# Performance work log

Hardware: AMD Instinct MI355X
Metric: run time of the kernel (lower is better)

## Reference

```python
import jax, jax.numpy as jnp
import numpy as np


def setup_inputs() -> dict:
    key = jax.random.key(0)
    k_x, k_q, k_k, k_v = jax.random.split(key, 4)
    seq_len, d_in, d_out = 4096, 1024, 1024
    x = jax.random.normal(k_x, (seq_len, d_in), dtype=jnp.float32)
    # torch nn.Linear weights are [d_out, d_in]; applied as x @ W.T
    scale = 1.0 / np.sqrt(d_in)
    Wq = jax.random.uniform(k_q, (d_out, d_in), jnp.float32, -scale, scale)
    Wk = jax.random.uniform(k_k, (d_out, d_in), jnp.float32, -scale, scale)
    Wv = jax.random.uniform(k_v, (d_out, d_in), jnp.float32, -scale, scale)
    return {"x": x, "Wq": Wq, "Wk": Wk, "Wv": Wv}


def reference(x, Wq, Wk, Wv):
    # x: [S, d_in]; Wq/Wk/Wv: [d_out, d_in]
    queries = x @ Wq.T          # [S, d_out]
    keys = x @ Wk.T             # [S, d_out]
    values = x @ Wv.T           # [S, d_out]
    d_k = keys.shape[-1]
    attn_scores = queries @ keys.T                      # [S, S]
    attn_weights = jax.nn.softmax(attn_scores / jnp.sqrt(jnp.float32(d_k)), axis=-1)
    S = attn_scores.shape[0]
    tril = jnp.tril(jnp.ones((S, S), dtype=attn_weights.dtype))
    masked = tril * attn_weights
    masked_norm = masked / jnp.sum(masked, axis=-1, keepdims=True)
    context_vec = masked_norm @ values                  # [S, d_out]
    return context_vec
```

## Files before the change

kernel.cpp:

```cpp
#include <hip/hip_runtime.h>
#include <hip/hip_bf16.h>


typedef __bf16 bf16_t;
typedef __bf16 bf16x4v __attribute__((ext_vector_type(4)));
typedef __bf16 bf16x8 __attribute__((ext_vector_type(8)));
typedef float f32x4 __attribute__((ext_vector_type(4)));
typedef unsigned char u8;
typedef long long i64_t;

#define AS1 __attribute__((address_space(1)))
#define AS3 __attribute__((address_space(3)))
#define WAIT_VMCNT(N) asm volatile("s_waitcnt vmcnt(" #N ")" ::: "memory")
#define BARRIER_RAW() asm volatile("s_barrier" ::: "memory")

__device__ __forceinline__ void async_copy16(const void* g, void* l) {
    __builtin_amdgcn_global_load_lds((AS1 void*)(g), (AS3 void*)(l), 16, 0, 0);
}

__device__ __forceinline__ u8 f32_to_fp8(float v) {
    return (u8)(__builtin_amdgcn_cvt_pk_fp8_f32(v, v, 0, false) & 0xff);
}

__device__ __forceinline__ void store_conv(float* p, float v) { *p = v; }
__device__ __forceinline__ void store_conv(bf16_t* p, float v) { *p = (bf16_t)v; }
__device__ __forceinline__ void store_conv(u8* p, float v) { *p = f32_to_fp8(v); }

__device__ __forceinline__ float sum32(const float* p) {
    const f32x4* v = (const f32x4*)p;
    float s = 0.f;
#pragma unroll
    for (int u = 0; u < 8; ++u) {
        f32x4 a = v[u];
        s += a[0] + a[1] + a[2] + a[3];
    }
    return s;
}

template <int EPI, typename OutT>
__device__ __forceinline__ void gemm_tile_bf16(const bf16_t* __restrict__ A, int lda,
                                               const bf16_t* __restrict__ B, int ldb,
                                               OutT* __restrict__ C, int ldc,
                                               int kb0, int kb1, float alpha,
                                               char* __restrict__ smem,
                                               const float* __restrict__ inv) {
    constexpr int BK = 64;
    bf16_t* As = (bf16_t*)smem;
    bf16_t* Bs = (bf16_t*)(smem + 32768);
    const int tid = threadIdx.x;
    const int lane = tid & 63, wave = tid >> 6;
    const int wm = wave >> 1, wn = wave & 1;
    const int q = lane >> 4, l16 = lane & 15;

    f32x4 acc[4][4] = {};

    const bf16_t* aSrc[4];
    const bf16_t* bSrc[4];
    int ldsOff[4];
#pragma unroll
    for (int it = 0; it < 4; ++it) {
        int c = it * 256 + tid;
        int r = c >> 3, b = c & 7;
        int sb = b ^ (r & 7);
        aSrc[it] = A + (size_t)r * lda + sb * 8;
        bSrc[it] = B + (size_t)r * ldb + sb * 8;
        ldsOff[it] = c * 8;
    }

    {
        const int k0 = kb0 * BK;
#pragma unroll
        for (int it = 0; it < 4; ++it) async_copy16(aSrc[it] + k0, &As[ldsOff[it]]);
#pragma unroll
        for (int it = 0; it < 4; ++it) async_copy16(bSrc[it] + k0, &Bs[ldsOff[it]]);
    }

    int cur = 0;
    for (int kb = kb0; kb < kb1; ++kb) {
        if (kb + 1 < kb1) {
            const int k0 = (kb + 1) * BK;
            const int boff = (cur ^ 1) * 8192;
#pragma unroll
            for (int it = 0; it < 4; ++it) async_copy16(aSrc[it] + k0, &As[boff + ldsOff[it]]);
#pragma unroll
            for (int it = 0; it < 4; ++it) async_copy16(bSrc[it] + k0, &Bs[boff + ldsOff[it]]);
            WAIT_VMCNT(8);
        } else {
            WAIT_VMCNT(0);
        }
        __builtin_amdgcn_sched_barrier(0);
        BARRIER_RAW();
        const bf16_t* Ab = As + cur * 8192;
        const bf16_t* Bb = Bs + cur * 8192;
        __builtin_amdgcn_s_setprio(1);
#pragma unroll
        for (int k2 = 0; k2 < 2; ++k2) {
            bf16x8 af[4], bfr[4];
#pragma unroll
            for (int mt = 0; mt < 4; ++mt) {
                int m = wm * 64 + mt * 16 + l16;
                int blk = (k2 * 4 + q) ^ (m & 7);
                af[mt] = *(const bf16x8*)&Ab[m * BK + blk * 8];
            }
#pragma unroll
            for (int nt = 0; nt < 4; ++nt) {
                int nn = wn * 64 + nt * 16 + l16;
                int blk = (k2 * 4 + q) ^ (nn & 7);
                bfr[nt] = *(const bf16x8*)&Bb[nn * BK + blk * 8];
            }
#pragma unroll
            for (int mt = 0; mt < 4; ++mt)
#pragma unroll
                for (int nt = 0; nt < 4; ++nt)
                    acc[mt][nt] = __builtin_amdgcn_mfma_f32_16x16x32_bf16(
                        af[mt], bfr[nt], acc[mt][nt], 0, 0, 0);
        }
        __builtin_amdgcn_s_setprio(0);
        BARRIER_RAW();
        cur ^= 1;
    }

    constexpr int S = (int)sizeof(OutT);
    constexpr int RB = 128 * S;
    const int row0 = wm * 64, col0 = wn * 64;
#pragma unroll
    for (int mt = 0; mt < 4; ++mt)
#pragma unroll
        for (int nt = 0; nt < 4; ++nt)
#pragma unroll
            for (int r = 0; r < 4; ++r) {
                int lr = row0 + mt * 16 + q * 4 + r;
                int lc = col0 + nt * 16 + l16;
                float v = acc[mt][nt][r];
                v = (EPI == 2) ? v * inv[lr] : v * alpha;
                int cb = (lc * S) >> 4;
                int sw = cb ^ ((lr >> 2) & 7);
                store_conv((OutT*)(smem + lr * RB + (sw << 4) + ((lc * S) & 15)), v);
            }
    __syncthreads();
#pragma unroll
    for (int p = 0; p < 4 * S; ++p) {
        int g = p * 4096 + tid * 16;
        int r = g / RB;
        int wb = g & (RB - 1);
        int sc = (wb >> 4) ^ ((r >> 2) & 7);
        f32x4 val = *(const f32x4*)(smem + r * RB + (sc << 4));
        *(f32x4*)((char*)C + (size_t)r * ((size_t)ldc * S) + wb) = val;
    }
}

__device__ __forceinline__ void gemm_tile_bf16_sb(const bf16_t* __restrict__ A, int lda,
                                                  const bf16_t* __restrict__ B, int ldb,
                                                  bf16_t* __restrict__ C, int ldc,
                                                  int kb1, char* __restrict__ smem) {
    constexpr int BK = 64;
    bf16_t* As = (bf16_t*)smem;
    bf16_t* Bs = (bf16_t*)(smem + 16384);
    const int tid = threadIdx.x;
    const int lane = tid & 63, wave = tid >> 6;
    const int wm = wave >> 1, wn = wave & 1;
    const int q = lane >> 4, l16 = lane & 15;

    f32x4 acc[4][4] = {};

    const bf16_t* aSrc[4];
    const bf16_t* bSrc[4];
    int ldsOff[4];
#pragma unroll
    for (int it = 0; it < 4; ++it) {
        int c = it * 256 + tid;
        int r = c >> 3, b = c & 7;
        int sb = b ^ (r & 7);
        aSrc[it] = A + (size_t)r * lda + sb * 8;
        bSrc[it] = B + (size_t)r * ldb + sb * 8;
        ldsOff[it] = c * 8;
    }

    for (int kb = 0; kb < kb1; ++kb) {
        const int k0 = kb * BK;
#pragma unroll
        for (int it = 0; it < 4; ++it) async_copy16(aSrc[it] + k0, &As[ldsOff[it]]);
#pragma unroll
        for (int it = 0; it < 4; ++it) async_copy16(bSrc[it] + k0, &Bs[ldsOff[it]]);
        __syncthreads();
        __builtin_amdgcn_s_setprio(1);
#pragma unroll
        for (int k2 = 0; k2 < 2; ++k2) {
            bf16x8 af[4], bfr[4];
#pragma unroll
            for (int mt = 0; mt < 4; ++mt) {
                int m = wm * 64 + mt * 16 + l16;
                int blk = (k2 * 4 + q) ^ (m & 7);
                af[mt] = *(const bf16x8*)&As[m * BK + blk * 8];
            }
#pragma unroll
            for (int nt = 0; nt < 4; ++nt) {
                int nn = wn * 64 + nt * 16 + l16;
                int blk = (k2 * 4 + q) ^ (nn & 7);
                bfr[nt] = *(const bf16x8*)&Bs[nn * BK + blk * 8];
            }
#pragma unroll
            for (int mt = 0; mt < 4; ++mt)
#pragma unroll
                for (int nt = 0; nt < 4; ++nt)
                    acc[mt][nt] = __builtin_amdgcn_mfma_f32_16x16x32_bf16(
                        af[mt], bfr[nt], acc[mt][nt], 0, 0, 0);
        }
        __builtin_amdgcn_s_setprio(0);
        __syncthreads();
    }

    constexpr int RB = 256;
    const int row0 = wm * 64, col0 = wn * 64;
#pragma unroll
    for (int mt = 0; mt < 4; ++mt)
#pragma unroll
        for (int nt = 0; nt < 4; ++nt)
#pragma unroll
            for (int r = 0; r < 4; ++r) {
                int lr = row0 + mt * 16 + q * 4 + r;
                int lc = col0 + nt * 16 + l16;
                int cb = (lc * 2) >> 4;
                int sw = cb ^ ((lr >> 2) & 7);
                *(bf16_t*)(smem + lr * RB + (sw << 4) + ((lc * 2) & 15)) =
                    (bf16_t)acc[mt][nt][r];
            }
    __syncthreads();
#pragma unroll
    for (int p = 0; p < 8; ++p) {
        int g = p * 4096 + tid * 16;
        int r = g >> 8, wb = g & 255;
        int sc = (wb >> 4) ^ ((r >> 2) & 7);
        f32x4 val = *(const f32x4*)(smem + r * RB + (sc << 4));
        *(f32x4*)((char*)C + (size_t)r * ((size_t)ldc * 2) + wb) = val;
    }
}

__device__ __forceinline__ void scores_tile_fp8_sb(const u8* __restrict__ A, int lda,
                                                   const u8* __restrict__ B, int ldb,
                                                   bf16_t* __restrict__ C, int ldc,
                                                   float alpha, char* __restrict__ smem,
                                                   float* __restrict__ partial,
                                                   int gr0, int gc0) {
    u8* As = (u8*)smem;
    u8* Bs = (u8*)(smem + 16384);
    const int tid = threadIdx.x;
    const int lane = tid & 63, wave = tid >> 6;
    const int wm = wave >> 1, wn = wave & 1;
    const int q = lane >> 4, l16 = lane & 15;

    f32x4 acc[4][4] = {};

    const u8* aSrc[4];
    const u8* bSrc[4];
    int ldsOff[4];
#pragma unroll
    for (int it = 0; it < 4; ++it) {
        int c = it * 256 + tid;
        int r = c >> 3, b = c & 7;
        int sb = b ^ (r & 7);
        aSrc[it] = A + (size_t)r * lda + sb * 16;
        bSrc[it] = B + (size_t)r * ldb + sb * 16;
        ldsOff[it] = c * 16;
    }

    for (int kb = 0; kb < 8; ++kb) {
        const int k0 = kb * 128;
#pragma unroll
        for (int it = 0; it < 4; ++it) async_copy16(aSrc[it] + k0, &As[ldsOff[it]]);
#pragma unroll
        for (int it = 0; it < 4; ++it) async_copy16(bSrc[it] + k0, &Bs[ldsOff[it]]);
        __syncthreads();
        __builtin_amdgcn_s_setprio(1);
#pragma unroll
        for (int k2 = 0; k2 < 4; ++k2) {
            i64_t af[4], bfr[4];
            const int cb = 2 * k2 + (q >> 1), co = (q & 1) * 8;
#pragma unroll
            for (int mt = 0; mt < 4; ++mt) {
                int m = wm * 64 + mt * 16 + l16;
                af[mt] = *(const i64_t*)&As[m * 128 + ((cb ^ (m & 7)) << 4) + co];
            }
#pragma unroll
            for (int nt = 0; nt < 4; ++nt) {
                int nn = wn * 64 + nt * 16 + l16;
                bfr[nt] = *(const i64_t*)&Bs[nn * 128 + ((cb ^ (nn & 7)) << 4) + co];
            }
#pragma unroll
            for (int mt = 0; mt < 4; ++mt)
#pragma unroll
                for (int nt = 0; nt < 4; ++nt)
                    acc[mt][nt] = __builtin_amdgcn_mfma_f32_16x16x32_fp8_fp8(
                        af[mt], bfr[nt], acc[mt][nt], 0, 0, 0);
        }
        __builtin_amdgcn_s_setprio(0);
        __syncthreads();
    }

    float* sred = (float*)(smem + 32768);
    const int row0 = wm * 64, col0 = wn * 64;
    float esum[4][4];
#pragma unroll
    for (int mt = 0; mt < 4; ++mt)
#pragma unroll
        for (int r = 0; r < 4; ++r) esum[mt][r] = 0.f;
#pragma unroll
    for (int mt = 0; mt < 4; ++mt)
#pragma unroll
        for (int nt = 0; nt < 4; ++nt)
#pragma unroll
            for (int r = 0; r < 4; ++r) {
                int lr = row0 + mt * 16 + q * 4 + r;
                int lc = col0 + nt * 16 + l16;
                float pe = (gc0 + lc > gr0 + lr) ? 0.f : __expf(acc[mt][nt][r] * alpha);
                esum[mt][r] += pe;
                int sw = (lc >> 3) ^ ((lr >> 2) & 7);
                *(bf16_t*)(smem + lr * 256 + (sw << 4) + ((lc * 2) & 15)) = (bf16_t)pe;
            }
#pragma unroll
    for (int mt = 0; mt < 4; ++mt)
#pragma unroll
        for (int r = 0; r < 4; ++r) {
#pragma unroll
            for (int off = 1; off < 16; off <<= 1)
                esum[mt][r] += __shfl_xor(esum[mt][r], off, 64);
            if (l16 == 0) sred[(row0 + mt * 16 + q * 4 + r) * 2 + wn] = esum[mt][r];
        }
    __syncthreads();
#pragma unroll
    for (int p = 0; p < 8; ++p) {
        int g = p * 4096 + tid * 16;
        int r = g >> 8;
        int wb = g & 255;
        int sc = (wb >> 4) ^ ((r >> 2) & 7);
        f32x4 val = *(const f32x4*)(smem + r * 256 + (sc << 4));
        *(f32x4*)((char*)C + (size_t)r * ((size_t)ldc * 2) + wb) = val;
    }
    if (tid < 128) partial[(size_t)tid * 32] = sred[tid * 2] + sred[tid * 2 + 1];
}

__global__ __launch_bounds__(256) void k_qkv(const bf16_t* __restrict__ xb,
                                             const bf16_t* __restrict__ wqk,
                                             u8* __restrict__ qk) {
    __shared__ __attribute__((aligned(16))) char smem[65536];
    int b = blockIdx.x;
    int bm = b & 31, bn = b >> 5;
    gemm_tile_bf16<0, u8>(xb + (size_t)bm * 128 * 1024, 1024,
                          wqk + (size_t)bn * 128 * 1024, 1024,
                          qk + (size_t)bm * 128 * 2048 + bn * 128, 2048,
                          0, 16, 1.f, smem, nullptr);
}

__global__ __launch_bounds__(256, 4) void k_sv(const bf16_t* __restrict__ xb,
                                               const bf16_t* __restrict__ wvb,
                                               const u8* __restrict__ qk,
                                               bf16_t* __restrict__ vt,
                                               bf16_t* __restrict__ P,
                                               float* __restrict__ rowsum_part) {
    __shared__ __attribute__((aligned(16))) char smem[33792];
    int b = blockIdx.x;
    if (b < 256) {
        int bm = b & 7, bn = b >> 3;
        gemm_tile_bf16_sb(wvb + (size_t)bm * 128 * 1024, 1024,
                          xb + (size_t)bn * 128 * 1024, 1024,
                          vt + (size_t)bm * 128 * 4096 + bn * 128, 4096,
                          16, smem);
        return;
    }
    int t = b - 256;
    int bm = (int)((sqrtf(8.f * (float)t + 1.f) - 1.f) * 0.5f);
    while (bm * (bm + 1) / 2 > t) --bm;
    while ((bm + 1) * (bm + 2) / 2 <= t) ++bm;
    int bn = t - bm * (bm + 1) / 2;
    scores_tile_fp8_sb(qk + (size_t)bm * 128 * 2048, 2048,
                       qk + 1024 + (size_t)bn * 128 * 2048, 2048,
                       P + (size_t)bm * 128 * 4096 + bn * 128, 4096,
                       0.03125f, smem,
                       rowsum_part + (size_t)bm * 128 * 32 + bn,
                       bm * 128, bn * 128);
    if (bn == bm) {
        float* rp = rowsum_part + (size_t)bm * 128 * 32;
        int tid = threadIdx.x;
        for (int r = tid >> 4; r < 128; r += 16)
            for (int u = bm + 1 + (tid & 15); u < 32; u += 16)
                rp[r * 32 + u] = 0.f;
    }
}

__global__ __launch_bounds__(256) void k_pv(const bf16_t* __restrict__ P,
                                            const bf16_t* __restrict__ vt,
                                            const float* __restrict__ rowsum_part,
                                            float* __restrict__ out,
                                            float* __restrict__ partials) {
    __shared__ __attribute__((aligned(16))) char smem[65536];
    __shared__ float sInv[128];
    int b = blockIdx.x;
    int bn = b & 7, g = b >> 3;
    int bm, s, ns;
    if (g < 11)      { bm = g;                  s = 0;             ns = 1; }
    else if (g < 33) { bm = 11 + (g - 11) / 2;  s = (g - 11) % 2;  ns = 2; }
    else             { bm = 22 + (g - 33) / 3;  s = (g - 33) % 3;  ns = 3; }
    int nk = 2 * (bm + 1);
    int kb0 = s * nk / ns;
    int kb1 = (s + 1) * nk / ns;

    const bf16_t* A = P + (size_t)bm * 128 * 4096;
    const bf16_t* B = vt + (size_t)bn * 128 * 4096;
    if (ns == 1) {
        int tid = threadIdx.x;
        if (tid < 128)
            sInv[tid] = 1.f / sum32(rowsum_part + (size_t)(bm * 128 + tid) * 32);
        gemm_tile_bf16<2, float>(A, 4096, B, 4096,
                                 out + (size_t)bm * 128 * 1024 + bn * 128, 1024,
                                 kb0, kb1, 1.f, smem, sInv);
    } else {
        int cum = (bm < 22) ? (bm - 11) * 2 : 22 + (bm - 22) * 3;
        gemm_tile_bf16<0, float>(A, 4096, B, 4096,
                                 partials + ((size_t)(cum + s) * 8 + bn) * 16384, 128,
                                 kb0, kb1, 1.f, smem, nullptr);
    }
}

__global__ __launch_bounds__(256) void k_reduce(const float* __restrict__ partials,
                                                const float* __restrict__ rowsum_part,
                                                float* __restrict__ out) {
    int b = blockIdx.x;
    int t = b % 168, p = b / 168;
    int bm = 11 + t % 21, bn = t / 21;
    int ns = (bm < 22) ? 2 : 3;
    int cum = (bm < 22) ? (bm - 11) * 2 : 22 + (bm - 22) * 3;
    __shared__ float sInv[8];
    int tid = threadIdx.x;
    if (tid < 8) {
        int row = bm * 128 + p * 8 + tid;
        sInv[tid] = 1.f / sum32(rowsum_part + (size_t)row * 32);
    }
    __syncthreads();

    int idx = p * 1024 + tid * 4;
    int lr = idx >> 7, lc = idx & 127;
    float sx = 0.f, sy = 0.f, sz = 0.f, sw = 0.f;
    for (int u = 0; u < ns; ++u) {
        const float4 v = *(const float4*)(partials + ((size_t)(cum + u) * 8 + bn) * 16384 + idx);
        sx += v.x; sy += v.y; sz += v.z; sw += v.w;
    }
    float inv = sInv[lr - p * 8];
    float4 o = {sx * inv, sy * inv, sz * inv, sw * inv};
    *(float4*)(out + (size_t)(bm * 128 + lr) * 1024 + bn * 128 + lc) = o;
}

__global__ __launch_bounds__(256) void cast_to_bf16(const float* __restrict__ x,
                                                    const float* __restrict__ Wq,
                                                    const float* __restrict__ Wk,
                                                    const float* __restrict__ Wv,
                                                    bf16_t* __restrict__ xb,
                                                    bf16_t* __restrict__ wqk,
                                                    bf16_t* __restrict__ wv) {
    const int NX = (4096 * 1024) / 4;
    const int NW = (1024 * 1024) / 4;
    int idx = blockIdx.x * 256 + threadIdx.x;
    const float* src;
    bf16_t* dst;
    int off;
    if (idx < NX) {
        src = x; dst = xb; off = idx;
    } else if (idx < NX + NW) {
        src = Wq; dst = wqk; off = idx - NX;
    } else if (idx < NX + 2 * NW) {
        src = Wk; dst = wqk + (size_t)NW * 4; off = idx - NX - NW;
    } else {
        src = Wv; dst = wv; off = idx - NX - 2 * NW;
    }
    float4 f = ((const float4*)src)[off];
    bf16x4v o;
    o.x = (bf16_t)f.x; o.y = (bf16_t)f.y; o.z = (bf16_t)f.z; o.w = (bf16_t)f.w;
    *(bf16x4v*)(dst + (size_t)off * 4) = o;
}

extern "C" void kernel_launch(void* const* d_in, const int* in_sizes, int n_in,
                              void* d_out, int out_size, void* d_ws, size_t ws_size,
                              hipStream_t stream) {
    (void)in_sizes; (void)n_in; (void)out_size; (void)ws_size;
    const float* x  = (const float*)d_in[0];
    const float* Wq = (const float*)d_in[1];
    const float* Wk = (const float*)d_in[2];
    const float* Wv = (const float*)d_in[3];
    float* out = (float*)d_out;

    char* ws = (char*)d_ws;
    bf16_t* xb   = (bf16_t*)(ws + (size_t)0);
    bf16_t* wqk  = (bf16_t*)(ws + ((size_t)8 << 20));
    bf16_t* wvb  = (bf16_t*)(ws + ((size_t)12 << 20));
    u8*     qk   = (u8*)(ws + ((size_t)14 << 20));
    bf16_t* vt   = (bf16_t*)(ws + ((size_t)22 << 20));
    bf16_t* P    = (bf16_t*)(ws + ((size_t)30 << 20));
    float* rowsp = (float*)(ws + ((size_t)62 << 20));
    float* parts = (float*)(ws + ((size_t)64 << 20));

    cast_to_bf16<<<7168, 256, 0, stream>>>(x, Wq, Wk, Wv, xb, wqk, wvb);

    k_qkv<<<512, 256, 0, stream>>>(xb, wqk, qk);

    k_sv<<<784, 256, 0, stream>>>(xb, wvb, qk, vt, P, rowsp);

    k_pv<<<504, 256, 0, stream>>>(P, vt, rowsp, out, parts);
    k_reduce<<<2688, 256, 0, stream>>>(parts, rowsp, out);
}
```

Measured before the change: 165.6 us.

## Use single-buffered 32KB-LDS PV tile for higher occupancy and finer split-K

Adds a single-buffered bf16 GEMM tile for the P·V stage that uses about 33KB of LDS instead of 64KB, and writes the fp32 epilogue in two 64-row halves so it fits that buffer. Launch bounds now request 4 blocks per CU. The split-K schedule is rebalanced to use up to 4 splits for the longest causal rows, which raises the block count and the matching reduce grid. In exchange, the kernel loses the overlap that double buffering gave between loads and MFMA, and writes more partial sums to memory for the reduce pass.

```diff
diff --git a/kernel.cpp b/kernel.cpp
--- a/kernel.cpp
+++ b/kernel.cpp
@@ -233,6 +233,103 @@
         int sc = (wb >> 4) ^ ((r >> 2) & 7);
         f32x4 val = *(const f32x4*)(smem + r * RB + (sc << 4));
         *(f32x4*)((char*)C + (size_t)r * ((size_t)ldc * 2) + wb) = val;
+    }
+}
+
+template <int EPI>
+__device__ __forceinline__ void gemm_tile_f32_sb(const bf16_t* __restrict__ A, int lda,
+                                                 const bf16_t* __restrict__ B, int ldb,
+                                                 float* __restrict__ C, int ldc,
+                                                 int kb0, int kb1,
+                                                 char* __restrict__ smem,
+                                                 const float* __restrict__ inv) {
+    constexpr int BK = 64;
+    bf16_t* As = (bf16_t*)smem;
+    bf16_t* Bs = (bf16_t*)(smem + 16384);
+    const int tid = threadIdx.x;
+    const int lane = tid & 63, wave = tid >> 6;
+    const int wm = wave >> 1, wn = wave & 1;
+    const int q = lane >> 4, l16 = lane & 15;
+
+    f32x4 acc[4][4] = {};
+
+    const bf16_t* aSrc[4];
+    const bf16_t* bSrc[4];
+    int ldsOff[4];
+#pragma unroll
+    for (int it = 0; it < 4; ++it) {
+        int c = it * 256 + tid;
+        int r = c >> 3, b = c & 7;
+        int sb = b ^ (r & 7);
+        aSrc[it] = A + (size_t)r * lda + sb * 8;
+        bSrc[it] = B + (size_t)r * ldb + sb * 8;
+        ldsOff[it] = c * 8;
+    }
+
+    for (int kb = kb0; kb < kb1; ++kb) {
+        const int k0 = kb * BK;
+#pragma unroll
+        for (int it = 0; it < 4; ++it) async_copy16(aSrc[it] + k0, &As[ldsOff[it]]);
+#pragma unroll
+        for (int it = 0; it < 4; ++it) async_copy16(bSrc[it] + k0, &Bs[ldsOff[it]]);
+        __syncthreads();
+        __builtin_amdgcn_s_setprio(1);
+#pragma unroll
+        for (int k2 = 0; k2 < 2; ++k2) {
+            bf16x8 af[4], bfr[4];
+#pragma unroll
+            for (int mt = 0; mt < 4; ++mt) {
+                int m = wm * 64 + mt * 16 + l16;
+                int blk = (k2 * 4 + q) ^ (m & 7);
+                af[mt] = *(const bf16x8*)&As[m * BK + blk * 8];
+            }
+#pragma unroll
+            for (int nt = 0; nt < 4; ++nt) {
+                int nn = wn * 64 + nt * 16 + l16;
+                int blk = (k2 * 4 + q) ^ (nn & 7);
+                bfr[nt] = *(const bf16x8*)&Bs[nn * BK + blk * 8];
+            }
+#pragma unroll
+            for (int mt = 0; mt < 4; ++mt)
+#pragma unroll
+                for (int nt = 0; nt < 4; ++nt)
+                    acc[mt][nt] = __builtin_amdgcn_mfma_f32_16x16x32_bf16(
+                        af[mt], bfr[nt], acc[mt][nt], 0, 0, 0);
+        }
+        __builtin_amdgcn_s_setprio(0);
+        __syncthreads();
+    }
+
+    const int row0 = wm * 64, col0 = wn * 64;
+#pragma unroll
+    for (int hh = 0; hh < 2; ++hh) {
+        if (wm == hh) {
+#pragma unroll
+            for (int mt = 0; mt < 4; ++mt)
+#pragma unroll
+                for (int nt = 0; nt < 4; ++nt)
+#pragma unroll
+                    for (int r = 0; r < 4; ++r) {
+                        int lr = row0 + mt * 16 + q * 4 + r;
+                        int rl = lr & 63;
+                        int lc = col0 + nt * 16 + l16;
+                        float v = acc[mt][nt][r];
+                        if (EPI == 2) v *= inv[lr];
+                        int cb = lc >> 2;
+                        int sw = cb ^ ((rl >> 2) & 7);
+                        *(float*)(smem + rl * 512 + (sw << 4) + ((lc * 4) & 15)) = v;
+                    }
+        }
+        __syncthreads();
+#pragma unroll
+        for (int p = 0; p < 8; ++p) {
+            int g = p * 4096 + tid * 16;
+            int r = g >> 9, wb = g & 511;
+            int sc = (wb >> 4) ^ ((r >> 2) & 7);
+            f32x4 val = *(const f32x4*)(smem + r * 512 + (sc << 4));
+            *(f32x4*)&C[(size_t)(hh * 64 + r) * ldc + (wb >> 2)] = val;
+        }
+        if (hh == 0) __syncthreads();
     }
 }
 
@@ -387,19 +484,20 @@
     }
 }
 
-__global__ __launch_bounds__(256) void k_pv(const bf16_t* __restrict__ P,
-                                            const bf16_t* __restrict__ vt,
-                                            const float* __restrict__ rowsum_part,
-                                            float* __restrict__ out,
-                                            float* __restrict__ partials) {
-    __shared__ __attribute__((aligned(16))) char smem[65536];
-    __shared__ float sInv[128];
+__global__ __launch_bounds__(256, 4) void k_pv(const bf16_t* __restrict__ P,
+                                               const bf16_t* __restrict__ vt,
+                                               const float* __restrict__ rowsum_part,
+                                               float* __restrict__ out,
+                                               float* __restrict__ partials) {
+    __shared__ __attribute__((aligned(16))) char smem[33792];
+    float* sInv = (float*)(smem + 32768);
     int b = blockIdx.x;
     int bn = b & 7, g = b >> 3;
     int bm, s, ns;
-    if (g < 11)      { bm = g;                  s = 0;             ns = 1; }
-    else if (g < 33) { bm = 11 + (g - 11) / 2;  s = (g - 11) % 2;  ns = 2; }
-    else             { bm = 22 + (g - 33) / 3;  s = (g - 33) % 3;  ns = 3; }
+    if (g < 8)       { bm = g;                 s = 0;            ns = 1; }
+    else if (g < 24) { bm = 8 + (g - 8) / 2;   s = (g - 8) % 2;  ns = 2; }
+    else if (g < 48) { bm = 16 + (g - 24) / 3; s = (g - 24) % 3; ns = 3; }
+    else             { bm = 24 + (g - 48) / 4; s = (g - 48) % 4; ns = 4; }
     int nk = 2 * (bm + 1);
     int kb0 = s * nk / ns;
     int kb1 = (s + 1) * nk / ns;
@@ -410,14 +508,16 @@
         int tid = threadIdx.x;
         if (tid < 128)
             sInv[tid] = 1.f / sum32(rowsum_part + (size_t)(bm * 128 + tid) * 32);
-        gemm_tile_bf16<2, float>(A, 4096, B, 4096,
-                                 out + (size_t)bm * 128 * 1024 + bn * 128, 1024,
-                                 kb0, kb1, 1.f, smem, sInv);
+        gemm_tile_f32_sb<2>(A, 4096, B, 4096,
+                            out + (size_t)bm * 128 * 1024 + bn * 128, 1024,
+                            kb0, kb1, smem, sInv);
     } else {
-        int cum = (bm < 22) ? (bm - 11) * 2 : 22 + (bm - 22) * 3;
-        gemm_tile_bf16<0, float>(A, 4096, B, 4096,
-                                 partials + ((size_t)(cum + s) * 8 + bn) * 16384, 128,
-                                 kb0, kb1, 1.f, smem, nullptr);
+        int cum = (bm < 16) ? (bm - 8) * 2
+                : (bm < 24) ? 16 + (bm - 16) * 3
+                            : 40 + (bm - 24) * 4;
+        gemm_tile_f32_sb<0>(A, 4096, B, 4096,
+                            partials + ((size_t)(cum + s) * 8 + bn) * 16384, 128,
+                            kb0, kb1, smem, nullptr);
     }
 }
 
@@ -425,10 +525,12 @@
                                                 const float* __restrict__ rowsum_part,
                                                 float* __restrict__ out) {
     int b = blockIdx.x;
-    int t = b % 168, p = b / 168;
-    int bm = 11 + t % 21, bn = t / 21;
-    int ns = (bm < 22) ? 2 : 3;
-    int cum = (bm < 22) ? (bm - 11) * 2 : 22 + (bm - 22) * 3;
+    int t = b % 192, p = b / 192;
+    int bm = t % 24 + 8, bn = t / 24;
+    int ns = (bm < 16) ? 2 : (bm < 24) ? 3 : 4;
+    int cum = (bm < 16) ? (bm - 8) * 2
+            : (bm < 24) ? 16 + (bm - 16) * 3
+                        : 40 + (bm - 24) * 4;
     __shared__ float sInv[8];
     int tid = threadIdx.x;
     if (tid < 8) {
@@ -503,6 +605,6 @@
 
     k_sv<<<784, 256, 0, stream>>>(xb, wvb, qk, vt, P, rowsp);
 
-    k_pv<<<504, 256, 0, stream>>>(P, vt, rowsp, out, parts);
-    k_reduce<<<2688, 256, 0, stream>>>(parts, rowsp, out);
-}
+    k_pv<<<640, 256, 0, stream>>>(P, vt, rowsp, out, parts);
+    k_reduce<<<3072, 256, 0, stream>>>(parts, rowsp, out);
+}
```

Measured after the change: 166.9 us. No clear change (+0.8%).
